# Optimization experiments

Measured on AMD Instinct MI355X. Metric: run time of the kernel, lower is better.

## Reference

```python
import jax, jax.numpy as jnp
import numpy as np

B, T, C, H = 4, 2048, 1024, 16
D = C // H
SCALE = D ** -0.5


def setup_inputs() -> dict:
    key = jax.random.key(0)
    ks = jax.random.split(key, 5)
    x = jax.random.normal(ks[0], (B, T, C), dtype=jnp.float32)
    key_padding_mask = jnp.zeros((B, T), dtype=bool)  # True = masked key
    W_qkv = jax.random.normal(ks[1], (C, 3 * C), dtype=jnp.float32) * (C ** -0.5)
    b_qkv = jax.random.normal(ks[2], (3 * C,), dtype=jnp.float32) * 0.02
    W_proj = jax.random.normal(ks[3], (C, C), dtype=jnp.float32) * (C ** -0.5)
    b_proj = jax.random.normal(ks[4], (C,), dtype=jnp.float32) * 0.02
    return {"x": x, "key_padding_mask": key_padding_mask, "W_qkv": W_qkv,
            "b_qkv": b_qkv, "W_proj": W_proj, "b_proj": b_proj}


def reference(x, key_padding_mask, W_qkv, b_qkv, W_proj, b_proj):
    Bx, Tx, Cx = x.shape
    qkv = x @ W_qkv + b_qkv                      # [B,T,3C]
    qkv = qkv.reshape(Bx, Tx, 3, H, D)
    q = jnp.transpose(qkv[:, :, 0], (0, 2, 1, 3))  # [B,H,T,D]
    k = jnp.transpose(qkv[:, :, 1], (0, 2, 1, 3))
    v = jnp.transpose(qkv[:, :, 2], (0, 2, 1, 3))
    attn = jnp.einsum('bhqd,bhkd->bhqk', q, k) * SCALE  # [B,H,T,T]
    causal = jnp.triu(jnp.ones((Tx, Tx), dtype=bool), k=1)  # True = masked
    neg_inf = jnp.finfo(attn.dtype).min
    attn = jnp.where(causal[None, None, :, :], neg_inf, attn)
    attn = jnp.where(key_padding_mask[:, None, None, :], neg_inf, attn)
    attn = jax.nn.softmax(attn, axis=-1)
    out = jnp.einsum('bhqk,bhkd->bhqd', attn, v)  # [B,H,T,D]
    out = jnp.transpose(out, (0, 2, 1, 3)).reshape(Bx, Tx, Cx)
    return out @ W_proj + b_proj
```

## Files before the change

kernel.cpp:

```cpp
#include <hip/hip_runtime.h>


typedef __bf16 bf16;
typedef __bf16 bf16x4 __attribute__((ext_vector_type(4)));
typedef __bf16 bf16x8 __attribute__((ext_vector_type(8)));
typedef float f32x4 __attribute__((ext_vector_type(4)));

#define MFMA(a, b, c) __builtin_amdgcn_mfma_f32_16x16x32_bf16((a), (b), (c), 0, 0, 0)

typedef const __attribute__((address_space(1))) void* gas_ptr;
typedef __attribute__((address_space(3))) void* las_ptr;

__device__ __forceinline__ void gload_lds16(const bf16* g, bf16* lds) {
  __builtin_amdgcn_global_load_lds((gas_ptr)g, (las_ptr)lds, 16, 0, 0);
}

__global__ __launch_bounds__(256) void k_cvt(const float* __restrict__ src,
                                             bf16* __restrict__ dst, int n4) {
  int i = blockIdx.x * 256 + threadIdx.x;
  if (i >= n4) return;
  float4 v = ((const float4*)src)[i];
  bf16x4 o = { (bf16)v.x, (bf16)v.y, (bf16)v.z, (bf16)v.w };
  ((bf16x4*)dst)[i] = o;
}

__global__ __launch_bounds__(256) void k_transpose(const float* __restrict__ src,
                                                   bf16* __restrict__ dst,
                                                   int R, int C) {
  __shared__ float tile[32][33];
  int c0 = blockIdx.x * 32, r0 = blockIdx.y * 32;
  int x = threadIdx.x & 31, y = threadIdx.x >> 5;
#pragma unroll
  for (int i = 0; i < 4; ++i)
    tile[y + i * 8][x] = src[(size_t)(r0 + y + i * 8) * C + (c0 + x)];
  __syncthreads();
#pragma unroll
  for (int i = 0; i < 4; ++i)
    dst[(size_t)(c0 + y + i * 8) * R + (r0 + x)] = (bf16)tile[x][y + i * 8];
}

__global__ void k_maskflags(const unsigned char* __restrict__ kpm,
                            int* __restrict__ flags) {
  int i = threadIdx.x;
  const uint4* p = (const uint4*)(kpm + i * 128);
  unsigned acc = 0;
#pragma unroll
  for (int j = 0; j < 8; ++j) { uint4 v = p[j]; acc |= v.x | v.y | v.z | v.w; }
  flags[i] = (acc != 0) ? 1 : 0;
}

template <int EPI>
__global__ __launch_bounds__(256, 2)
void k_gemm_bt(const bf16* __restrict__ A, const bf16* __restrict__ Bt,
               const float* __restrict__ bias, float* __restrict__ fout,
               bf16* __restrict__ qp, bf16* __restrict__ kp,
               bf16* __restrict__ vtp, int M, int N, int K) {
  __shared__ bf16 Ab[2][128 * 32];
  __shared__ bf16 Bb[2][128 * 32];
  const int tid = threadIdx.x;
  const int wave = tid >> 6, lane = tid & 63;
  const int m0 = blockIdx.x * 128, n0 = blockIdx.y * 128;
  const int wr = wave >> 1, wc = wave & 1;
  const int lrow = lane & 15, kb = (lane >> 4) * 8;
  f32x4 acc[4][4] = {};
  const int nkt = K >> 5;

  auto stage = [&](int buf, int kt) {
#pragma unroll
    for (int i = 0; i < 2; ++i) {
      int c = i * 4 + wave;
      const bf16* ga = A + (size_t)(m0 + c * 16 + (lane >> 2)) * K + kt * 32 + (lane & 3) * 8;
      gload_lds16(ga, &Ab[buf][c * 512]);
      const bf16* gb = Bt + (size_t)(n0 + c * 16 + (lane >> 2)) * K + kt * 32 + (lane & 3) * 8;
      gload_lds16(gb, &Bb[buf][c * 512]);
    }
  };

  stage(0, 0);
  asm volatile("s_waitcnt vmcnt(0)" ::: "memory");
  __syncthreads();
  int cur = 0;
  for (int kt = 0; kt < nkt; ++kt) {
    if (kt + 1 < nkt) stage(cur ^ 1, kt + 1);
    bf16x8 af[4], bfr[4];
#pragma unroll
    for (int m = 0; m < 4; ++m)
      af[m] = *(const bf16x8*)&Ab[cur][(wr * 64 + m * 16 + lrow) * 32 + kb];
#pragma unroll
    for (int n = 0; n < 4; ++n)
      bfr[n] = *(const bf16x8*)&Bb[cur][(wc * 64 + n * 16 + lrow) * 32 + kb];
#pragma unroll
    for (int m = 0; m < 4; ++m)
#pragma unroll
      for (int n = 0; n < 4; ++n)
        acc[m][n] = MFMA(af[m], bfr[n], acc[m][n]);
    asm volatile("s_waitcnt vmcnt(0)" ::: "memory");
    __syncthreads();
    cur ^= 1;
  }

#pragma unroll
  for (int m = 0; m < 4; ++m) {
#pragma unroll
    for (int n = 0; n < 4; ++n) {
      const int col = n0 + wc * 64 + n * 16 + lrow;
      const int row0 = m0 + wr * 64 + m * 16 + (lane >> 4) * 4;
      const float bv = bias[col];
      if (EPI == 0) {
        const int which = col >> 10;
        const int h = (col >> 6) & 15, d = col & 63;
        const int b = row0 >> 11, t0 = row0 & 2047;
        const int bh = b * 16 + h;
        if (which == 2) {
          bf16x4 pk;
#pragma unroll
          for (int j = 0; j < 4; ++j) pk[j] = (bf16)(acc[m][n][j] + bv);
          *(bf16x4*)&vtp[((size_t)bh * 64 + d) * 2048 + t0] = pk;
        } else {
          bf16* dstp = (which == 0) ? qp : kp;
          const float sc = (which == 0) ? 0.18033688011112042f : 1.0f;
#pragma unroll
          for (int j = 0; j < 4; ++j)
            dstp[((size_t)bh * 2048 + (t0 + j)) * 64 + d] = (bf16)((acc[m][n][j] + bv) * sc);
        }
      } else {
#pragma unroll
        for (int j = 0; j < 4; ++j)
          fout[(size_t)(row0 + j) * N + col] = acc[m][n][j] + bv;
      }
    }
  }
}

__global__ __launch_bounds__(256, 2)
void k_flash(const bf16* __restrict__ Q, const bf16* __restrict__ Kg,
             const bf16* __restrict__ Vt, const unsigned char* __restrict__ kpm,
             const int* __restrict__ tflags, bf16* __restrict__ O) {
  const int bh = blockIdx.x;
  const int b = bh >> 4, h = bh & 15;
  const int w = blockIdx.y;
  const int tid = threadIdx.x, wave = tid >> 6, lane = tid & 63;
  const int lrow = lane & 15, g = lane >> 4;

  __shared__ bf16 Kt[2][128 * 64];
  __shared__ bf16 Vts[64 * 128];
  __shared__ bf16 PT[4][2][2048];

  const bf16* Kbh = Kg + (size_t)bh * 2048 * 64;
  const bf16* Vbh = Vt + (size_t)bh * 64 * 2048;

  const int k_src_col = (((lane & 7) ^ (lane >> 3)) << 3);
  const int k_row_in_chunk = lane >> 3;

  const int ptb2 = g * 256 + lrow * 8;

  auto stageK = [&](int buf, int kvt) {
#pragma unroll
    for (int i = 0; i < 4; ++i) {
      int c = i * 4 + wave;
      gload_lds16(Kbh + (size_t)(kvt * 128 + c * 8 + k_row_in_chunk) * 64 + k_src_col,
                  &Kt[buf][c * 512]);
    }
  };
  auto stageV = [&](int kvt) {
#pragma unroll
    for (int i = 0; i < 4; ++i) {
      int c = i * 4 + wave;
      int vs = (((lane & 15) ^ (((c & 1) << 2) | g)) << 3);
      gload_lds16(Vbh + (size_t)(c * 4 + g) * 2048 + kvt * 128 + vs, &Vts[c * 512]);
    }
  };

  int cur = 0;
  for (int pass = 0; pass < 2; ++pass) {
    const int qt = pass ? (15 - w) : w;

    const bf16* Qbase = Q + ((size_t)bh * 2048 + qt * 128 + wave * 32) * 64;
    bf16x8 qf[2][2];
#pragma unroll
    for (int m = 0; m < 2; ++m)
#pragma unroll
      for (int ks = 0; ks < 2; ++ks)
        qf[m][ks] = *(const bf16x8*)&Qbase[(m * 16 + lrow) * 64 + ks * 32 + g * 8];

    f32x4 oacc[2][4] = {};
    float rm[2][4], rl[2][4];
#pragma unroll
    for (int m = 0; m < 2; ++m)
#pragma unroll
      for (int j = 0; j < 4; ++j) { rm[m][j] = -1e30f; rl[m][j] = 0.f; }

    stageK(cur, 0);
    asm volatile("s_waitcnt vmcnt(0)" ::: "memory");
    __builtin_amdgcn_s_barrier();
    __builtin_amdgcn_sched_barrier(0);

    for (int kvt = 0; kvt <= qt; ++kvt) {
      const bool pref = (kvt < qt);
      stageV(kvt);
      if (pref) stageK(cur ^ 1, kvt + 1);

      f32x4 s[2][8];
#pragma unroll
      for (int n = 0; n < 8; ++n) {
        const int row = n * 16 + lrow;
        bf16x8 kf0 = *(const bf16x8*)&Kt[cur][row * 64 + ((g ^ (lrow & 7)) << 3)];
        bf16x8 kf1 = *(const bf16x8*)&Kt[cur][row * 64 + (((4 + g) ^ (lrow & 7)) << 3)];
#pragma unroll
        for (int m = 0; m < 2; ++m) {
          f32x4 t = {};
          t = MFMA(qf[m][0], kf0, t);
          t = MFMA(qf[m][1], kf1, t);
          s[m][n] = t;
        }
      }

      if (tflags[b * 16 + kvt]) {
#pragma unroll
        for (int n = 0; n < 8; ++n) {
          const int col = kvt * 128 + n * 16 + lrow;
          if (kpm[b * 2048 + col]) {
#pragma unroll
            for (int m = 0; m < 2; ++m)
#pragma unroll
              for (int j = 0; j < 4; ++j) s[m][n][j] = -1e30f;
          }
        }
      }
      if (kvt == qt) {
#pragma unroll
        for (int n = 0; n < 8; ++n) {
          const int col = n * 16 + lrow;
#pragma unroll
          for (int m = 0; m < 2; ++m)
#pragma unroll
            for (int j = 0; j < 4; ++j) {
              const int row = wave * 32 + m * 16 + g * 4 + j;
              if (col > row) s[m][n][j] = -1e30f;
            }
        }
      }

      float tmax[2][4];
#pragma unroll
      for (int m = 0; m < 2; ++m)
#pragma unroll
        for (int j = 0; j < 4; ++j) {
          float v01 = fmaxf(s[m][0][j], s[m][1][j]);
          float v23 = fmaxf(s[m][2][j], s[m][3][j]);
          float v45 = fmaxf(s[m][4][j], s[m][5][j]);
          float v67 = fmaxf(s[m][6][j], s[m][7][j]);
          tmax[m][j] = fmaxf(fmaxf(v01, v23), fmaxf(v45, v67));
        }
#pragma unroll
      for (int off = 1; off < 16; off <<= 1)
#pragma unroll
        for (int m = 0; m < 2; ++m)
#pragma unroll
          for (int j = 0; j < 4; ++j)
            tmax[m][j] = fmaxf(tmax[m][j], __shfl_xor(tmax[m][j], off, 64));

      bool need = false;
#pragma unroll
      for (int m = 0; m < 2; ++m)
#pragma unroll
        for (int j = 0; j < 4; ++j) need |= (tmax[m][j] > rm[m][j] + 8.f);
      if (__any(need)) {
#pragma unroll
        for (int m = 0; m < 2; ++m)
#pragma unroll
          for (int j = 0; j < 4; ++j) {
            const float mn = fmaxf(rm[m][j], tmax[m][j]);
            const float f = exp2f(rm[m][j] - mn);
            rm[m][j] = mn;
            rl[m][j] *= f;
#pragma unroll
            for (int nt = 0; nt < 4; ++nt) oacc[m][nt][j] *= f;
          }
      }

#pragma unroll
      for (int m = 0; m < 2; ++m)
#pragma unroll
        for (int n = 0; n < 8; ++n) {
          bf16x4 pk;
#pragma unroll
          for (int j = 0; j < 4; ++j) {
            const float p = exp2f(s[m][n][j] - rm[m][j]);
            rl[m][j] += p;
            pk[j] = (bf16)p;
          }
          const int woff = (n * 16 + lrow) * 32 + g * 8;
          *(bf16x4*)((char*)&PT[wave][m][0] + woff) = pk;
        }

      if (pref) asm volatile("s_waitcnt vmcnt(4)" ::: "memory");
      else      asm volatile("s_waitcnt vmcnt(0)" ::: "memory");
      __builtin_amdgcn_s_barrier();
      __builtin_amdgcn_sched_barrier(0);

#pragma unroll
      for (int ks = 0; ks < 4; ++ks) {
        bf16x4 plo[2], phi[2];
#pragma unroll
        for (int m = 0; m < 2; ++m) {
          las_ptr pa_ = (las_ptr)((char*)&PT[wave][m][0] + ptb2);
          asm volatile("ds_read_b64_tr_b16 %0, %1 offset:%2"
                       : "=v"(plo[m]) : "v"(pa_), "i"(ks * 1024));
          asm volatile("ds_read_b64_tr_b16 %0, %1 offset:%2"
                       : "=v"(phi[m]) : "v"(pa_), "i"(ks * 1024 + 128));
        }
        bf16x8 vf[4];
#pragma unroll
        for (int nt = 0; nt < 4; ++nt) {
          const int d = nt * 16 + lrow;
          vf[nt] = *(const bf16x8*)((const char*)Vts + d * 256 +
                                    (((ks * 4 + g) ^ (lrow & 7)) << 4));
        }
        asm volatile("s_waitcnt lgkmcnt(0)" ::: "memory");
        __builtin_amdgcn_sched_barrier(0);
#pragma unroll
        for (int nt = 0; nt < 4; ++nt)
#pragma unroll
          for (int m = 0; m < 2; ++m) {
            bf16x8 pa = __builtin_shufflevector(plo[m], phi[m], 0, 1, 2, 3, 4, 5, 6, 7);
            oacc[m][nt] = MFMA(pa, vf[nt], oacc[m][nt]);
          }
      }

      asm volatile("s_waitcnt vmcnt(0)" ::: "memory");
      __builtin_amdgcn_s_barrier();
      __builtin_amdgcn_sched_barrier(0);
      cur ^= 1;
    }

#pragma unroll
    for (int off = 1; off < 16; off <<= 1)
#pragma unroll
      for (int m = 0; m < 2; ++m)
#pragma unroll
        for (int j = 0; j < 4; ++j) rl[m][j] += __shfl_xor(rl[m][j], off, 64);

#pragma unroll
    for (int m = 0; m < 2; ++m)
#pragma unroll
      for (int nt = 0; nt < 4; ++nt)
#pragma unroll
        for (int j = 0; j < 4; ++j) {
          const int t = qt * 128 + wave * 32 + m * 16 + g * 4 + j;
          const int c = h * 64 + nt * 16 + lrow;
          O[((size_t)b * 2048 + t) * 1024 + c] = (bf16)(oacc[m][nt][j] / rl[m][j]);
        }
  }
}

extern "C" void kernel_launch(void* const* d_in, const int* in_sizes, int n_in,
                              void* d_out, int out_size, void* d_ws, size_t ws_size,
                              hipStream_t stream) {
  const float* x = (const float*)d_in[0];
  const unsigned char* kpm = (const unsigned char*)d_in[1];
  const float* Wqkv = (const float*)d_in[2];
  const float* bqkv = (const float*)d_in[3];
  const float* Wproj = (const float*)d_in[4];
  const float* bproj = (const float*)d_in[5];
  float* out = (float*)d_out;
  char* ws = (char*)d_ws;

  bf16* xb     = (bf16*)(ws + 0);
  bf16* WqkvT  = (bf16*)(ws + 16777216);
  bf16* WprojT = (bf16*)(ws + 23068672);
  bf16* Qb     = (bf16*)(ws + 25165824);
  bf16* Kb     = (bf16*)(ws + 41943040);
  bf16* Vtb    = (bf16*)(ws + 58720256);
  bf16* AOb    = (bf16*)(ws + 75497472);
  int*  tflags = (int*)(ws + 0);

  k_cvt<<<8192, 256, 0, stream>>>(x, xb, 2097152);
  k_transpose<<<dim3(96, 32), 256, 0, stream>>>(Wqkv, WqkvT, 1024, 3072);
  k_transpose<<<dim3(32, 32), 256, 0, stream>>>(Wproj, WprojT, 1024, 1024);
  k_gemm_bt<0><<<dim3(64, 24), 256, 0, stream>>>(xb, WqkvT, bqkv, nullptr, Qb, Kb,
                                                 Vtb, 8192, 3072, 1024);
  k_maskflags<<<1, 64, 0, stream>>>(kpm, tflags);
  k_flash<<<dim3(64, 8), 256, 0, stream>>>(Qb, Kb, Vtb, kpm, tflags, AOb);
  k_gemm_bt<1><<<dim3(64, 8), 256, 0, stream>>>(AOb, WprojT, bproj, out, nullptr,
                                                nullptr, nullptr, 8192, 1024, 1024);
}
```

Measured before the change: 201.7 us.

## Pre-pack K/V into MFMA fragment layout and load directly from global

The QKV GEMM epilogue now writes K and V in a packed, fragment-ordered layout, so each lane's 16-byte operand is contiguous in memory. The attention kernel then reads K and V fragments straight from global memory (L2) instead of staging them through LDS. This removes the K/V shared buffers and the per-tile barriers, and raises the occupancy hint to 4 blocks per CU. The cost is that each wave now loads K/V redundantly and there is no explicit prefetch, so global-load latency is hidden only by the extra occupancy.

```diff
diff --git a/kernel.cpp b/kernel.cpp
--- a/kernel.cpp
+++ b/kernel.cpp
@@ -115,13 +115,22 @@
           bf16x4 pk;
 #pragma unroll
           for (int j = 0; j < 4; ++j) pk[j] = (bf16)(acc[m][n][j] + bv);
-          *(bf16x4*)&vtp[((size_t)bh * 64 + d) * 2048 + t0] = pk;
+          const size_t idx = (((size_t)bh * 64 + (t0 >> 5)) * 4 + (d >> 4)) * 512 +
+                             ((((t0 >> 3) & 3) * 16 + (d & 15)) * 8) + (t0 & 7);
+          *(bf16x4*)&vtp[idx] = pk;
+        } else if (which == 1) {
+#pragma unroll
+          for (int j = 0; j < 4; ++j) {
+            const int t = t0 + j;
+            const size_t idx = (((size_t)bh * 128 + (t >> 4)) * 2 + (d >> 5)) * 512 +
+                               ((((d >> 3) & 3) * 16 + (t & 15)) * 8) + (d & 7);
+            kp[idx] = (bf16)(acc[m][n][j] + bv);
+          }
         } else {
-          bf16* dstp = (which == 0) ? qp : kp;
-          const float sc = (which == 0) ? 0.18033688011112042f : 1.0f;
 #pragma unroll
           for (int j = 0; j < 4; ++j)
-            dstp[((size_t)bh * 2048 + (t0 + j)) * 64 + d] = (bf16)((acc[m][n][j] + bv) * sc);
+            qp[((size_t)bh * 2048 + (t0 + j)) * 64 + d] =
+                (bf16)((acc[m][n][j] + bv) * 0.18033688011112042f);
         }
       } else {
 #pragma unroll
@@ -132,9 +141,9 @@
   }
 }
 
-__global__ __launch_bounds__(256, 2)
-void k_flash(const bf16* __restrict__ Q, const bf16* __restrict__ Kg,
-             const bf16* __restrict__ Vt, const unsigned char* __restrict__ kpm,
+__global__ __launch_bounds__(256, 4)
+void k_flash(const bf16* __restrict__ Q, const bf16* __restrict__ Kp,
+             const bf16* __restrict__ Vp, const unsigned char* __restrict__ kpm,
              const int* __restrict__ tflags, bf16* __restrict__ O) {
   const int bh = blockIdx.x;
   const int b = bh >> 4, h = bh & 15;
@@ -142,36 +151,13 @@
   const int tid = threadIdx.x, wave = tid >> 6, lane = tid & 63;
   const int lrow = lane & 15, g = lane >> 4;
 
-  __shared__ bf16 Kt[2][128 * 64];
-  __shared__ bf16 Vts[64 * 128];
   __shared__ bf16 PT[4][2][2048];
 
-  const bf16* Kbh = Kg + (size_t)bh * 2048 * 64;
-  const bf16* Vbh = Vt + (size_t)bh * 64 * 2048;
-
-  const int k_src_col = (((lane & 7) ^ (lane >> 3)) << 3);
-  const int k_row_in_chunk = lane >> 3;
+  const bf16* Kbh = Kp + (size_t)bh * 131072;
+  const bf16* Vbh = Vp + (size_t)bh * 131072;
 
   const int ptb2 = g * 256 + lrow * 8;
 
-  auto stageK = [&](int buf, int kvt) {
-#pragma unroll
-    for (int i = 0; i < 4; ++i) {
-      int c = i * 4 + wave;
-      gload_lds16(Kbh + (size_t)(kvt * 128 + c * 8 + k_row_in_chunk) * 64 + k_src_col,
-                  &Kt[buf][c * 512]);
-    }
-  };
-  auto stageV = [&](int kvt) {
-#pragma unroll
-    for (int i = 0; i < 4; ++i) {
-      int c = i * 4 + wave;
-      int vs = (((lane & 15) ^ (((c & 1) << 2) | g)) << 3);
-      gload_lds16(Vbh + (size_t)(c * 4 + g) * 2048 + kvt * 128 + vs, &Vts[c * 512]);
-    }
-  };
-
-  int cur = 0;
   for (int pass = 0; pass < 2; ++pass) {
     const int qt = pass ? (15 - w) : w;
 
@@ -190,22 +176,13 @@
 #pragma unroll
       for (int j = 0; j < 4; ++j) { rm[m][j] = -1e30f; rl[m][j] = 0.f; }
 
-    stageK(cur, 0);
-    asm volatile("s_waitcnt vmcnt(0)" ::: "memory");
-    __builtin_amdgcn_s_barrier();
-    __builtin_amdgcn_sched_barrier(0);
-
     for (int kvt = 0; kvt <= qt; ++kvt) {
-      const bool pref = (kvt < qt);
-      stageV(kvt);
-      if (pref) stageK(cur ^ 1, kvt + 1);
-
       f32x4 s[2][8];
 #pragma unroll
       for (int n = 0; n < 8; ++n) {
-        const int row = n * 16 + lrow;
-        bf16x8 kf0 = *(const bf16x8*)&Kt[cur][row * 64 + ((g ^ (lrow & 7)) << 3)];
-        bf16x8 kf1 = *(const bf16x8*)&Kt[cur][row * 64 + (((4 + g) ^ (lrow & 7)) << 3)];
+        const bf16* kbase = Kbh + (size_t)(kvt * 8 + n) * 1024 + lane * 8;
+        bf16x8 kf0 = *(const bf16x8*)(kbase);
+        bf16x8 kf1 = *(const bf16x8*)(kbase + 512);
 #pragma unroll
         for (int m = 0; m < 2; ++m) {
           f32x4 t = {};
@@ -294,11 +271,8 @@
           *(bf16x4*)((char*)&PT[wave][m][0] + woff) = pk;
         }
 
-      if (pref) asm volatile("s_waitcnt vmcnt(4)" ::: "memory");
-      else      asm volatile("s_waitcnt vmcnt(0)" ::: "memory");
-      __builtin_amdgcn_s_barrier();
+      asm volatile("s_waitcnt lgkmcnt(0)" ::: "memory");
       __builtin_amdgcn_sched_barrier(0);
-
 #pragma unroll
       for (int ks = 0; ks < 4; ++ks) {
         bf16x4 plo[2], phi[2];
@@ -311,12 +285,10 @@
                        : "=v"(phi[m]) : "v"(pa_), "i"(ks * 1024 + 128));
         }
         bf16x8 vf[4];
-#pragma unroll
-        for (int nt = 0; nt < 4; ++nt) {
-          const int d = nt * 16 + lrow;
-          vf[nt] = *(const bf16x8*)((const char*)Vts + d * 256 +
-                                    (((ks * 4 + g) ^ (lrow & 7)) << 4));
-        }
+        const bf16* vbase = Vbh + (size_t)(kvt * 4 + ks) * 2048 + lane * 8;
+#pragma unroll
+        for (int nt = 0; nt < 4; ++nt)
+          vf[nt] = *(const bf16x8*)(vbase + nt * 512);
         asm volatile("s_waitcnt lgkmcnt(0)" ::: "memory");
         __builtin_amdgcn_sched_barrier(0);
 #pragma unroll
@@ -327,11 +299,6 @@
             oacc[m][nt] = MFMA(pa, vf[nt], oacc[m][nt]);
           }
       }
-
-      asm volatile("s_waitcnt vmcnt(0)" ::: "memory");
-      __builtin_amdgcn_s_barrier();
-      __builtin_amdgcn_sched_barrier(0);
-      cur ^= 1;
     }
 
 #pragma unroll
```

After: 296.1 us. 1.47x slower.

## Shrink flash KV tile to 64, drop double-buffering, raise occupancy to 4 blocks

Applied to the files above, without the earlier changes.

The flash attention kernel moves from 128-wide KV tiles with double-buffered K staging to 64-wide single-buffered K/V tiles, cutting LDS use so four blocks can be resident per CU. Waves whose query rows lie entirely above a diagonal 64-key tile skip its compute, and MFMA sections are bracketed with s_setprio to favour matrix issue. The cost is that global-to-LDS loads are no longer overlapped within a block, so each iteration waits on its loads behind a barrier, and the smaller tiles mean twice as many barriers and softmax rescale checks per KV range.

```diff
diff --git a/kernel.cpp b/kernel.cpp
--- a/kernel.cpp
+++ b/kernel.cpp
@@ -132,7 +132,7 @@
   }
 }
 
-__global__ __launch_bounds__(256, 2)
+__global__ __launch_bounds__(256, 4)
 void k_flash(const bf16* __restrict__ Q, const bf16* __restrict__ Kg,
              const bf16* __restrict__ Vt, const unsigned char* __restrict__ kpm,
              const int* __restrict__ tflags, bf16* __restrict__ O) {
@@ -142,36 +142,18 @@
   const int tid = threadIdx.x, wave = tid >> 6, lane = tid & 63;
   const int lrow = lane & 15, g = lane >> 4;
 
-  __shared__ bf16 Kt[2][128 * 64];
-  __shared__ bf16 Vts[64 * 128];
-  __shared__ bf16 PT[4][2][2048];
+  __shared__ bf16 Kt[64 * 64];
+  __shared__ bf16 Vts[64 * 64];
+  __shared__ bf16 PT[4][2][1024];
 
   const bf16* Kbh = Kg + (size_t)bh * 2048 * 64;
   const bf16* Vbh = Vt + (size_t)bh * 64 * 2048;
 
-  const int k_src_col = (((lane & 7) ^ (lane >> 3)) << 3);
-  const int k_row_in_chunk = lane >> 3;
+  const int src_sw = (((lane & 7) ^ (lane >> 3)) << 3);
+  const int rowc = lane >> 3;
 
   const int ptb2 = g * 256 + lrow * 8;
 
-  auto stageK = [&](int buf, int kvt) {
-#pragma unroll
-    for (int i = 0; i < 4; ++i) {
-      int c = i * 4 + wave;
-      gload_lds16(Kbh + (size_t)(kvt * 128 + c * 8 + k_row_in_chunk) * 64 + k_src_col,
-                  &Kt[buf][c * 512]);
-    }
-  };
-  auto stageV = [&](int kvt) {
-#pragma unroll
-    for (int i = 0; i < 4; ++i) {
-      int c = i * 4 + wave;
-      int vs = (((lane & 15) ^ (((c & 1) << 2) | g)) << 3);
-      gload_lds16(Vbh + (size_t)(c * 4 + g) * 2048 + kvt * 128 + vs, &Vts[c * 512]);
-    }
-  };
-
-  int cur = 0;
   for (int pass = 0; pass < 2; ++pass) {
     const int qt = pass ? (15 - w) : w;
 
@@ -190,148 +172,155 @@
 #pragma unroll
       for (int j = 0; j < 4; ++j) { rm[m][j] = -1e30f; rl[m][j] = 0.f; }
 
-    stageK(cur, 0);
-    asm volatile("s_waitcnt vmcnt(0)" ::: "memory");
-    __builtin_amdgcn_s_barrier();
-    __builtin_amdgcn_sched_barrier(0);
-
-    for (int kvt = 0; kvt <= qt; ++kvt) {
-      const bool pref = (kvt < qt);
-      stageV(kvt);
-      if (pref) stageK(cur ^ 1, kvt + 1);
-
-      f32x4 s[2][8];
-#pragma unroll
-      for (int n = 0; n < 8; ++n) {
-        const int row = n * 16 + lrow;
-        bf16x8 kf0 = *(const bf16x8*)&Kt[cur][row * 64 + ((g ^ (lrow & 7)) << 3)];
-        bf16x8 kf1 = *(const bf16x8*)&Kt[cur][row * 64 + (((4 + g) ^ (lrow & 7)) << 3)];
-#pragma unroll
-        for (int m = 0; m < 2; ++m) {
-          f32x4 t = {};
-          t = MFMA(qf[m][0], kf0, t);
-          t = MFMA(qf[m][1], kf1, t);
-          s[m][n] = t;
-        }
+    const int nkt = 2 * qt + 2;
+    const int wlimit = 2 * qt + (wave >> 1);
+
+    for (int kt = 0; kt < nkt; ++kt) {
+#pragma unroll
+      for (int i = 0; i < 2; ++i) {
+        int c = i * 4 + wave;
+        gload_lds16(Kbh + (size_t)(kt * 64 + c * 8 + rowc) * 64 + src_sw, &Kt[c * 512]);
       }
-
-      if (tflags[b * 16 + kvt]) {
-#pragma unroll
-        for (int n = 0; n < 8; ++n) {
-          const int col = kvt * 128 + n * 16 + lrow;
-          if (kpm[b * 2048 + col]) {
-#pragma unroll
-            for (int m = 0; m < 2; ++m)
-#pragma unroll
-              for (int j = 0; j < 4; ++j) s[m][n][j] = -1e30f;
-          }
-        }
+#pragma unroll
+      for (int i = 0; i < 2; ++i) {
+        int c = i * 4 + wave;
+        gload_lds16(Vbh + (size_t)(c * 8 + rowc) * 2048 + kt * 64 + src_sw, &Vts[c * 512]);
       }
-      if (kvt == qt) {
-#pragma unroll
-        for (int n = 0; n < 8; ++n) {
-          const int col = n * 16 + lrow;
-#pragma unroll
-          for (int m = 0; m < 2; ++m)
-#pragma unroll
-            for (int j = 0; j < 4; ++j) {
-              const int row = wave * 32 + m * 16 + g * 4 + j;
-              if (col > row) s[m][n][j] = -1e30f;
-            }
-        }
-      }
-
-      float tmax[2][4];
-#pragma unroll
-      for (int m = 0; m < 2; ++m)
-#pragma unroll
-        for (int j = 0; j < 4; ++j) {
-          float v01 = fmaxf(s[m][0][j], s[m][1][j]);
-          float v23 = fmaxf(s[m][2][j], s[m][3][j]);
-          float v45 = fmaxf(s[m][4][j], s[m][5][j]);
-          float v67 = fmaxf(s[m][6][j], s[m][7][j]);
-          tmax[m][j] = fmaxf(fmaxf(v01, v23), fmaxf(v45, v67));
-        }
-#pragma unroll
-      for (int off = 1; off < 16; off <<= 1)
-#pragma unroll
-        for (int m = 0; m < 2; ++m)
-#pragma unroll
-          for (int j = 0; j < 4; ++j)
-            tmax[m][j] = fmaxf(tmax[m][j], __shfl_xor(tmax[m][j], off, 64));
-
-      bool need = false;
-#pragma unroll
-      for (int m = 0; m < 2; ++m)
-#pragma unroll
-        for (int j = 0; j < 4; ++j) need |= (tmax[m][j] > rm[m][j] + 8.f);
-      if (__any(need)) {
-#pragma unroll
-        for (int m = 0; m < 2; ++m)
-#pragma unroll
-          for (int j = 0; j < 4; ++j) {
-            const float mn = fmaxf(rm[m][j], tmax[m][j]);
-            const float f = exp2f(rm[m][j] - mn);
-            rm[m][j] = mn;
-            rl[m][j] *= f;
-#pragma unroll
-            for (int nt = 0; nt < 4; ++nt) oacc[m][nt][j] *= f;
-          }
-      }
-
-#pragma unroll
-      for (int m = 0; m < 2; ++m)
-#pragma unroll
-        for (int n = 0; n < 8; ++n) {
-          bf16x4 pk;
-#pragma unroll
-          for (int j = 0; j < 4; ++j) {
-            const float p = exp2f(s[m][n][j] - rm[m][j]);
-            rl[m][j] += p;
-            pk[j] = (bf16)p;
-          }
-          const int woff = (n * 16 + lrow) * 32 + g * 8;
-          *(bf16x4*)((char*)&PT[wave][m][0] + woff) = pk;
-        }
-
-      if (pref) asm volatile("s_waitcnt vmcnt(4)" ::: "memory");
-      else      asm volatile("s_waitcnt vmcnt(0)" ::: "memory");
-      __builtin_amdgcn_s_barrier();
-      __builtin_amdgcn_sched_barrier(0);
-
-#pragma unroll
-      for (int ks = 0; ks < 4; ++ks) {
-        bf16x4 plo[2], phi[2];
-#pragma unroll
-        for (int m = 0; m < 2; ++m) {
-          las_ptr pa_ = (las_ptr)((char*)&PT[wave][m][0] + ptb2);
-          asm volatile("ds_read_b64_tr_b16 %0, %1 offset:%2"
-                       : "=v"(plo[m]) : "v"(pa_), "i"(ks * 1024));
-          asm volatile("ds_read_b64_tr_b16 %0, %1 offset:%2"
-                       : "=v"(phi[m]) : "v"(pa_), "i"(ks * 1024 + 128));
-        }
-        bf16x8 vf[4];
-#pragma unroll
-        for (int nt = 0; nt < 4; ++nt) {
-          const int d = nt * 16 + lrow;
-          vf[nt] = *(const bf16x8*)((const char*)Vts + d * 256 +
-                                    (((ks * 4 + g) ^ (lrow & 7)) << 4));
-        }
-        asm volatile("s_waitcnt lgkmcnt(0)" ::: "memory");
-        __builtin_amdgcn_sched_barrier(0);
-#pragma unroll
-        for (int nt = 0; nt < 4; ++nt)
-#pragma unroll
-          for (int m = 0; m < 2; ++m) {
-            bf16x8 pa = __builtin_shufflevector(plo[m], phi[m], 0, 1, 2, 3, 4, 5, 6, 7);
-            oacc[m][nt] = MFMA(pa, vf[nt], oacc[m][nt]);
-          }
-      }
-
       asm volatile("s_waitcnt vmcnt(0)" ::: "memory");
       __builtin_amdgcn_s_barrier();
       __builtin_amdgcn_sched_barrier(0);
-      cur ^= 1;
+
+      if (kt <= wlimit) {
+        f32x4 s[2][4];
+        __builtin_amdgcn_s_setprio(1);
+#pragma unroll
+        for (int n = 0; n < 4; ++n) {
+          const int row = n * 16 + lrow;
+          bf16x8 kf0 = *(const bf16x8*)&Kt[row * 64 + ((g ^ (lrow & 7)) << 3)];
+          bf16x8 kf1 = *(const bf16x8*)&Kt[row * 64 + (((4 + g) ^ (lrow & 7)) << 3)];
+#pragma unroll
+          for (int m = 0; m < 2; ++m) {
+            f32x4 t = {};
+            t = MFMA(qf[m][0], kf0, t);
+            t = MFMA(qf[m][1], kf1, t);
+            s[m][n] = t;
+          }
+        }
+        __builtin_amdgcn_s_setprio(0);
+
+        if (tflags[b * 16 + (kt >> 1)]) {
+#pragma unroll
+          for (int n = 0; n < 4; ++n) {
+            const int col = kt * 64 + n * 16 + lrow;
+            if (kpm[b * 2048 + col]) {
+#pragma unroll
+              for (int m = 0; m < 2; ++m)
+#pragma unroll
+                for (int j = 0; j < 4; ++j) s[m][n][j] = -1e30f;
+            }
+          }
+        }
+        if (kt >= 2 * qt) {
+#pragma unroll
+          for (int n = 0; n < 4; ++n) {
+            const int ccol = (kt - 2 * qt) * 64 + n * 16 + lrow;
+#pragma unroll
+            for (int m = 0; m < 2; ++m)
+#pragma unroll
+              for (int j = 0; j < 4; ++j) {
+                const int crow = wave * 32 + m * 16 + g * 4 + j;
+                if (ccol > crow) s[m][n][j] = -1e30f;
+              }
+          }
+        }
+
+        float tmax[2][4];
+#pragma unroll
+        for (int m = 0; m < 2; ++m)
+#pragma unroll
+          for (int j = 0; j < 4; ++j) {
+            float v01 = fmaxf(s[m][0][j], s[m][1][j]);
+            float v23 = fmaxf(s[m][2][j], s[m][3][j]);
+            tmax[m][j] = fmaxf(v01, v23);
+          }
+#pragma unroll
+        for (int off = 1; off < 16; off <<= 1)
+#pragma unroll
+          for (int m = 0; m < 2; ++m)
+#pragma unroll
+            for (int j = 0; j < 4; ++j)
+              tmax[m][j] = fmaxf(tmax[m][j], __shfl_xor(tmax[m][j], off, 64));
+
+        bool need = false;
+#pragma unroll
+        for (int m = 0; m < 2; ++m)
+#pragma unroll
+          for (int j = 0; j < 4; ++j) need |= (tmax[m][j] > rm[m][j] + 8.f);
+        if (__any(need)) {
+#pragma unroll
+          for (int m = 0; m < 2; ++m)
+#pragma unroll
+            for (int j = 0; j < 4; ++j) {
+              const float mn = fmaxf(rm[m][j], tmax[m][j]);
+              const float f = exp2f(rm[m][j] - mn);
+              rm[m][j] = mn;
+              rl[m][j] *= f;
+#pragma unroll
+              for (int nt = 0; nt < 4; ++nt) oacc[m][nt][j] *= f;
+            }
+        }
+
+#pragma unroll
+        for (int m = 0; m < 2; ++m)
+#pragma unroll
+          for (int n = 0; n < 4; ++n) {
+            bf16x4 pk;
+#pragma unroll
+            for (int j = 0; j < 4; ++j) {
+              const float p = exp2f(s[m][n][j] - rm[m][j]);
+              rl[m][j] += p;
+              pk[j] = (bf16)p;
+            }
+            const int woff = (n * 16 + lrow) * 32 + g * 8;
+            *(bf16x4*)((char*)&PT[wave][m][0] + woff) = pk;
+          }
+
+        asm volatile("s_waitcnt lgkmcnt(0)" ::: "memory");
+        __builtin_amdgcn_sched_barrier(0);
+#pragma unroll
+        for (int ks = 0; ks < 2; ++ks) {
+          bf16x4 plo[2], phi[2];
+#pragma unroll
+          for (int m = 0; m < 2; ++m) {
+            las_ptr pa_ = (las_ptr)((char*)&PT[wave][m][0] + ptb2);
+            asm volatile("ds_read_b64_tr_b16 %0, %1 offset:%2"
+                         : "=v"(plo[m]) : "v"(pa_), "i"(ks * 1024));
+            asm volatile("ds_read_b64_tr_b16 %0, %1 offset:%2"
+                         : "=v"(phi[m]) : "v"(pa_), "i"(ks * 1024 + 128));
+          }
+          bf16x8 vf[4];
+#pragma unroll
+          for (int nt = 0; nt < 4; ++nt) {
+            const int d = nt * 16 + lrow;
+            vf[nt] = *(const bf16x8*)((const char*)Vts + d * 128 +
+                                      (((ks * 4 + g) ^ (lrow & 7)) << 4));
+          }
+          asm volatile("s_waitcnt lgkmcnt(0)" ::: "memory");
+          __builtin_amdgcn_sched_barrier(0);
+          __builtin_amdgcn_s_setprio(1);
+#pragma unroll
+          for (int nt = 0; nt < 4; ++nt)
+#pragma unroll
+            for (int m = 0; m < 2; ++m) {
+              bf16x8 pa = __builtin_shufflevector(plo[m], phi[m], 0, 1, 2, 3, 4, 5, 6, 7);
+              oacc[m][nt] = MFMA(pa, vf[nt], oacc[m][nt]);
+            }
+          __builtin_amdgcn_s_setprio(0);
+        }
+      }
+
+      __builtin_amdgcn_s_barrier();
+      __builtin_amdgcn_sched_barrier(0);
     }
 
 #pragma unroll
```

Result: slower. 225.2 us (+11.7%).
